# Performance work log

Hardware: AMD Instinct MI355X
Metric: run time of the kernel (lower is better)

## Reference

```python
import jax, jax.numpy as jnp
import numpy as np

N = 50000
E = 800000
D = 128
H = 8
HD = D // H


def setup_inputs() -> dict:
    key = jax.random.key(0)
    ks = jax.random.split(key, 12)
    s = 1.0 / np.sqrt(D)
    x = jax.random.normal(ks[0], (N, D), dtype=jnp.float32)
    edge_index = jax.random.randint(ks[1], (2, E), 0, N, dtype=jnp.int64)
    edge_bias = jax.random.normal(ks[2], (E, H), dtype=jnp.float32)
    Wq = jax.random.uniform(ks[3], (D, D), jnp.float32, -s, s)
    bq = jax.random.uniform(ks[4], (D,), jnp.float32, -s, s)
    Wk = jax.random.uniform(ks[5], (D, D), jnp.float32, -s, s)
    bk = jax.random.uniform(ks[6], (D,), jnp.float32, -s, s)
    Wv = jax.random.uniform(ks[7], (D, D), jnp.float32, -s, s)
    bv = jax.random.uniform(ks[8], (D,), jnp.float32, -s, s)
    Wo = jax.random.uniform(ks[9], (D, D), jnp.float32, -s, s)
    bo = jax.random.uniform(ks[10], (D,), jnp.float32, -s, s)
    return {"x": x, "edge_index": edge_index, "edge_bias": edge_bias,
            "Wq": Wq, "bq": bq, "Wk": Wk, "bk": bk,
            "Wv": Wv, "bv": bv, "Wo": Wo, "bo": bo}


def reference(x, edge_index, edge_bias, Wq, bq, Wk, bk, Wv, bv, Wo, bo):
    scale = HD ** -0.5
    row, col = edge_index[0], edge_index[1]
    # Node-level projections -> [N, H, HD]
    q = (x @ Wq + bq).reshape(N, H, HD)
    k = (x @ Wk + bk).reshape(N, H, HD)
    v = (x @ Wv + bv).reshape(N, H, HD)
    # Edge-level gather + per-edge attention logits [E, H]
    q_i = q[col]
    k_j = k[row]
    v_j = v[row]
    attn = jnp.einsum('ehd,ehd->eh', q_i, k_j) * scale + edge_bias
    # Scatter-softmax over incoming edges of each destination node (col)
    seg_max = jax.ops.segment_max(attn, col, num_segments=N)  # [N, H]
    seg_max = jnp.where(jnp.isfinite(seg_max), seg_max, 0.0)  # empty segments -> 0
    ex = jnp.exp(attn - seg_max[col])
    denom = jax.ops.segment_sum(ex, col, num_segments=N)      # [N, H]
    attn = ex / (denom[col] + 1e-16)
    # Scatter-add weighted values -> [N, H, HD]
    weighted_v = attn[:, :, None] * v_j
    out = jax.ops.segment_sum(weighted_v, col, num_segments=N)
    out = out.reshape(N, D)
    return out @ Wo + bo
```

## Files before the change

kernel.cpp:

```cpp
#include <hip/hip_runtime.h>
#include <math.h>

#define NN 50000
#define EE 800000
#define DD 128
#define HH 8
#define HDD 16
#define CAP 64

typedef __attribute__((ext_vector_type(8))) short short8;
typedef __attribute__((ext_vector_type(4))) float f32x4;

union U8 { ushort u[8]; int4 v; short8 s; };

__device__ __forceinline__ ushort f2bf(float f) {
    uint u = __float_as_uint(f);
    uint r = (u + 0x7fffu + ((u >> 16) & 1u)) >> 16;
    return (ushort)r;
}
__device__ __forceinline__ float bf2f(ushort u) {
    return __uint_as_float(((uint)u) << 16);
}

__global__ void k_prep(const float* __restrict__ Wq, const float* __restrict__ Wk,
                       const float* __restrict__ Wv, const float* __restrict__ Wo,
                       const float* __restrict__ bq, const float* __restrict__ bk,
                       const float* __restrict__ bv, const float* __restrict__ bo,
                       ushort* __restrict__ Wt, float* __restrict__ bpack,
                       int* __restrict__ cursor) {
    if (blockIdx.x < 256) {
        int tid = blockIdx.x * 256 + threadIdx.x;
        int w = tid >> 14, rem = tid & 16383, c = rem >> 7, i = rem & 127;
        const float* W = (w == 0) ? Wq : (w == 1) ? Wk : (w == 2) ? Wv : Wo;
        float s = (w == 0) ? 0.25f : 1.0f;
        Wt[(size_t)w * 16384 + c * 128 + i] = f2bf(W[i * 128 + c] * s);
        if (i == 0) {
            const float* B = (w == 0) ? bq : (w == 1) ? bk : (w == 2) ? bv : bo;
            bpack[w * 128 + c] = B[c] * s;
        }
    } else {
        int i = (blockIdx.x - 256) * 256 + threadIdx.x;
        if (i < NN) cursor[i] = 0;
    }
}

__global__ void k_fill(const int* __restrict__ col, const int* __restrict__ row,
                       int* __restrict__ cursor, int2* __restrict__ reB) {
    int e = blockIdx.x * blockDim.x + threadIdx.x;
    if (e >= EE) return;
    int c = col[e];
    int p = atomicAdd(&cursor[c], 1);
    if (p < CAP) reB[(size_t)c * CAP + p] = make_int2(row[e], e);
}

#define PAD 136

__global__ __launch_bounds__(256) void k_qkv3(
    const float* __restrict__ x, const ushort* __restrict__ Wt,
    const float* __restrict__ bpk,
    ushort* __restrict__ qb, ushort* __restrict__ kk, ushort* __restrict__ vv) {
    __shared__ ushort lA[128 * PAD];
    __shared__ ushort lB[128 * PAD];
    int tid = threadIdx.x;
    int lane = tid & 63, wave = tid >> 6;
    int r0 = blockIdx.x * 128;

#pragma unroll
    for (int it = 0; it < 8; it++) {
        int slot = it * 256 + tid;
        int arow = slot >> 4, c8 = slot & 15;
        int ar = min(r0 + arow, NN - 1);
        const float* xp = x + (size_t)ar * 128 + c8 * 8;
        float4 a = *(const float4*)xp;
        float4 b = *(const float4*)(xp + 4);
        U8 r;
        r.u[0] = f2bf(a.x); r.u[1] = f2bf(a.y); r.u[2] = f2bf(a.z); r.u[3] = f2bf(a.w);
        r.u[4] = f2bf(b.x); r.u[5] = f2bf(b.y); r.u[6] = f2bf(b.z); r.u[7] = f2bf(b.w);
        *(int4*)&lA[arow * PAD + c8 * 8] = r.v;
    }

    int wm = wave >> 1, wn = wave & 1;
    int lr = lane & 15, lg = lane >> 4;

    for (int w = 0; w < 3; w++) {
#pragma unroll
        for (int it = 0; it < 8; it++) {
            int slot = it * 256 + tid;
            int brow = slot >> 4, c16 = slot & 15;
            *(int4*)&lB[brow * PAD + c16 * 8] =
                *(const int4*)&Wt[(size_t)w * 16384 + brow * 128 + c16 * 8];
        }
        __syncthreads();

        f32x4 acc[4][4];
#pragma unroll
        for (int m = 0; m < 4; m++)
#pragma unroll
            for (int n = 0; n < 4; n++) acc[m][n] = (f32x4){0.f, 0.f, 0.f, 0.f};

#pragma unroll
        for (int ks = 0; ks < 4; ks++) {
            short8 a[4], b[4];
#pragma unroll
            for (int m = 0; m < 4; m++)
                a[m] = *(const short8*)&lA[(wm * 64 + m * 16 + lr) * PAD + ks * 32 + lg * 8];
#pragma unroll
            for (int n = 0; n < 4; n++)
                b[n] = *(const short8*)&lB[(wn * 64 + n * 16 + lr) * PAD + ks * 32 + lg * 8];
#pragma unroll
            for (int m = 0; m < 4; m++)
#pragma unroll
                for (int n = 0; n < 4; n++)
                    acc[m][n] = __builtin_amdgcn_mfma_f32_16x16x32_bf16(a[m], b[n], acc[m][n], 0, 0, 0);
        }

#pragma unroll
        for (int n = 0; n < 4; n++) {
            int gcol = wn * 64 + n * 16 + lr;
            float bv_ = bpk[w * 128 + gcol];
#pragma unroll
            for (int m = 0; m < 4; m++) {
#pragma unroll
                for (int rg = 0; rg < 4; rg++) {
                    int grow = r0 + wm * 64 + m * 16 + lg * 4 + rg;
                    if (grow < NN) {
                        float val = acc[m][n][rg] + bv_;
                        ushort h16 = f2bf(val);
                        if (w == 0)      qb[(size_t)grow * 128 + gcol] = h16;
                        else if (w == 1) kk[(size_t)grow * 128 + gcol] = h16;
                        else             vv[(size_t)grow * 128 + gcol] = h16;
                    }
                }
            }
        }
        __syncthreads();
    }
}

__global__ __launch_bounds__(256) void k_gemm128(
    const ushort* __restrict__ A, const ushort* __restrict__ Bt,
    const float* __restrict__ bias, float* __restrict__ Cf, int M) {
    __shared__ ushort lA[128 * PAD];
    __shared__ ushort lB[128 * PAD];
    int tid = threadIdx.x;
    int lane = tid & 63, wave = tid >> 6;
    int r0 = blockIdx.x * 128;

#pragma unroll
    for (int it = 0; it < 8; it++) {
        int slot = it * 256 + tid;
        int row = slot >> 4, c16 = slot & 15;
        int ar = min(r0 + row, M - 1);
        *(int4*)&lA[row * PAD + c16 * 8] = *(const int4*)&A[(size_t)ar * 128 + c16 * 8];
        *(int4*)&lB[row * PAD + c16 * 8] = *(const int4*)&Bt[row * 128 + c16 * 8];
    }
    __syncthreads();

    int wm = wave >> 1, wn = wave & 1;
    int lr = lane & 15, lg = lane >> 4;
    f32x4 acc[4][4];
#pragma unroll
    for (int m = 0; m < 4; m++)
#pragma unroll
        for (int n = 0; n < 4; n++) acc[m][n] = (f32x4){0.f, 0.f, 0.f, 0.f};

#pragma unroll
    for (int ks = 0; ks < 4; ks++) {
        short8 a[4], b[4];
#pragma unroll
        for (int m = 0; m < 4; m++)
            a[m] = *(const short8*)&lA[(wm * 64 + m * 16 + lr) * PAD + ks * 32 + lg * 8];
#pragma unroll
        for (int n = 0; n < 4; n++)
            b[n] = *(const short8*)&lB[(wn * 64 + n * 16 + lr) * PAD + ks * 32 + lg * 8];
#pragma unroll
        for (int m = 0; m < 4; m++)
#pragma unroll
            for (int n = 0; n < 4; n++)
                acc[m][n] = __builtin_amdgcn_mfma_f32_16x16x32_bf16(a[m], b[n], acc[m][n], 0, 0, 0);
    }

#pragma unroll
    for (int n = 0; n < 4; n++) {
        int gcol = wn * 64 + n * 16 + lr;
        float bv_ = bias[gcol];
#pragma unroll
        for (int m = 0; m < 4; m++) {
#pragma unroll
            for (int rg = 0; rg < 4; rg++) {
                int grow = r0 + wm * 64 + m * 16 + lg * 4 + rg;
                if (grow < M) Cf[(size_t)grow * 128 + gcol] = acc[m][n][rg] + bv_;
            }
        }
    }
}

__global__ __launch_bounds__(256) void k_attn(
    const ushort* __restrict__ qb, const ushort* __restrict__ kk,
    const ushort* __restrict__ vv, const float* __restrict__ ebias,
    const int2* __restrict__ reB, const int* __restrict__ deg,
    ushort* __restrict__ aggb) {
    int wave = threadIdx.x >> 6;
    int lane = threadIdx.x & 63;
    int n = blockIdx.x * 4 + wave;
    if (n >= NN) return;
    int cnt = min(deg[n], CAP);
    const int2* bucket = reB + (size_t)n * CAP;
    int h = lane >> 3;
    int j = lane & 7;
    int hb = lane & ~7;

    float qf[16];
    {
        U8 q0, q1;
        const ushort* qp = qb + (size_t)n * DD + h * HDD;
        q0.v = *(const int4*)qp;
        q1.v = *(const int4*)(qp + 8);
#pragma unroll
        for (int t = 0; t < 8; t++) qf[t] = bf2f(q0.u[t]);
#pragma unroll
        for (int t = 0; t < 8; t++) qf[8 + t] = bf2f(q1.u[t]);
    }

    float m = -INFINITY;
    float denom = 0.f;
    float acc0 = 0.f, acc1 = 0.f;

    for (int idx = 0; idx < cnt; idx += 8) {
        int my = idx + j;
        bool valid = my < cnt;
        int2 re = valid ? bucket[my] : make_int2(0, 0);
        int r = re.x;
        float logit = -INFINITY;
        if (valid) {
            const ushort* kp = kk + (size_t)r * DD + h * HDD;
            U8 a0, a1;
            a0.v = *(const int4*)kp;
            a1.v = *(const int4*)(kp + 8);
            float d = 0.f;
#pragma unroll
            for (int t = 0; t < 8; t++) d += qf[t] * bf2f(a0.u[t]);
#pragma unroll
            for (int t = 0; t < 8; t++) d += qf[8 + t] * bf2f(a1.u[t]);
            logit = d + ebias[(size_t)re.y * HH + h];
        }
        float cm = logit;
        cm = fmaxf(cm, __shfl_xor(cm, 1));
        cm = fmaxf(cm, __shfl_xor(cm, 2));
        cm = fmaxf(cm, __shfl_xor(cm, 4));
        float mnew = fmaxf(m, cm);
        float sc = __expf(m - mnew);
        float p = __expf(logit - mnew);
        m = mnew;
        float ps = p;
        ps += __shfl_xor(ps, 1);
        ps += __shfl_xor(ps, 2);
        ps += __shfl_xor(ps, 4);
        denom = denom * sc + ps;
        acc0 *= sc;
        acc1 *= sc;
#pragma unroll
        for (int j2 = 0; j2 < 8; j2++) {
            float pj = __shfl(p, hb + j2);
            int rj = __shfl(r, hb + j2);
            uint vp = *(const uint*)(vv + (size_t)rj * DD + 2 * lane);
            acc0 += pj * bf2f((ushort)(vp & 0xffffu));
            acc1 += pj * bf2f((ushort)(vp >> 16));
        }
    }
    float inv = 1.0f / (denom + 1e-16f);
    uint pack = (uint)f2bf(acc0 * inv) | ((uint)f2bf(acc1 * inv) << 16);
    *(uint*)&aggb[(size_t)n * DD + 2 * lane] = pack;
}

extern "C" void kernel_launch(void* const* d_in, const int* in_sizes, int n_in,
                              void* d_out, int out_size, void* d_ws, size_t ws_size,
                              hipStream_t stream) {
    const float* x     = (const float*)d_in[0];
    const int*   eidx  = (const int*)d_in[1];
    const float* ebias = (const float*)d_in[2];
    const float* Wq    = (const float*)d_in[3];
    const float* bq    = (const float*)d_in[4];
    const float* Wk    = (const float*)d_in[5];
    const float* bk    = (const float*)d_in[6];
    const float* Wv    = (const float*)d_in[7];
    const float* bv    = (const float*)d_in[8];
    const float* Wo    = (const float*)d_in[9];
    const float* bo    = (const float*)d_in[10];
    float* out = (float*)d_out;

    const int* row = eidx;
    const int* col = eidx + EE;

    char* p = (char*)d_ws;
    ushort* qb    = (ushort*)p;  p += (size_t)NN * DD * 2;
    ushort* kk    = (ushort*)p;  p += (size_t)NN * DD * 2;
    ushort* vvp   = (ushort*)p;  p += (size_t)NN * DD * 2;
    ushort* aggb  = (ushort*)p;  p += (size_t)NN * DD * 2;
    ushort* Wt    = (ushort*)p;  p += (size_t)4 * 16384 * 2;
    float*  bpk   = (float*)p;   p += 4 * 128 * 4;
    int2*   reB   = (int2*)p;    p += (size_t)NN * CAP * 8;
    int* cursor   = (int*)p;     p += (size_t)NN * 4;

    const int SCB = (NN + 255) / 256;

    hipLaunchKernelGGL(k_prep, dim3(256 + SCB), dim3(256), 0, stream,
                       Wq, Wk, Wv, Wo, bq, bk, bv, bo, Wt, bpk, cursor);
    hipLaunchKernelGGL(k_fill, dim3((EE + 255) / 256), dim3(256), 0, stream,
                       col, row, cursor, reB);

    const int GB = (NN + 127) / 128;
    hipLaunchKernelGGL(k_qkv3, dim3(GB), dim3(256), 0, stream,
                       x, Wt, bpk, qb, kk, vvp);

    hipLaunchKernelGGL(k_attn, dim3(NN / 4), dim3(256), 0, stream,
                       qb, kk, vvp, ebias, reB, cursor, aggb);

    hipLaunchKernelGGL(k_gemm128, dim3(GB), dim3(256), 0, stream,
                       aggb, Wt + 3 * 16384, bpk + 3 * 128, out, NN);
}
```

Before: 212.4 us.

## Fuse edge bucketing into QKV GEMM and output projection into attention

Edge bucketing (atomic fill) now runs as extra blocks of the QKV projection kernel instead of a separate launch. The output projection by Wo is fused into the attention kernel: each block stages Wo as bf16 in LDS and runs a persistent loop over nodes, doing a per-node 128x128 matvec with scalar FMAs from LDS. This removes two launches and the aggb round trip, but replaces an MFMA GEMM with scalar matvec work per node and caps the attention grid at 1024 persistent blocks, which may lower occupancy for the latency-bound gather.

```diff
diff --git a/kernel.cpp b/kernel.cpp
--- a/kernel.cpp
+++ b/kernel.cpp
@@ -7,6 +7,10 @@
 #define HH 8
 #define HDD 16
 #define CAP 64
+#define GB 391
+#define FILLB 3125
+#define PAD 136
+#define WOP 132
 
 typedef __attribute__((ext_vector_type(8))) short short8;
 typedef __attribute__((ext_vector_type(4))) float f32x4;
@@ -23,45 +27,47 @@
 }
 
 __global__ void k_prep(const float* __restrict__ Wq, const float* __restrict__ Wk,
-                       const float* __restrict__ Wv, const float* __restrict__ Wo,
+                       const float* __restrict__ Wv,
                        const float* __restrict__ bq, const float* __restrict__ bk,
-                       const float* __restrict__ bv, const float* __restrict__ bo,
+                       const float* __restrict__ bv,
                        ushort* __restrict__ Wt, float* __restrict__ bpack,
                        int* __restrict__ cursor) {
-    if (blockIdx.x < 256) {
+    if (blockIdx.x < 192) {
         int tid = blockIdx.x * 256 + threadIdx.x;
         int w = tid >> 14, rem = tid & 16383, c = rem >> 7, i = rem & 127;
-        const float* W = (w == 0) ? Wq : (w == 1) ? Wk : (w == 2) ? Wv : Wo;
+        const float* W = (w == 0) ? Wq : (w == 1) ? Wk : Wv;
         float s = (w == 0) ? 0.25f : 1.0f;
         Wt[(size_t)w * 16384 + c * 128 + i] = f2bf(W[i * 128 + c] * s);
         if (i == 0) {
-            const float* B = (w == 0) ? bq : (w == 1) ? bk : (w == 2) ? bv : bo;
+            const float* B = (w == 0) ? bq : (w == 1) ? bk : bv;
             bpack[w * 128 + c] = B[c] * s;
         }
     } else {
-        int i = (blockIdx.x - 256) * 256 + threadIdx.x;
+        int i = (blockIdx.x - 192) * 256 + threadIdx.x;
         if (i < NN) cursor[i] = 0;
     }
 }
 
-__global__ void k_fill(const int* __restrict__ col, const int* __restrict__ row,
-                       int* __restrict__ cursor, int2* __restrict__ reB) {
-    int e = blockIdx.x * blockDim.x + threadIdx.x;
-    if (e >= EE) return;
-    int c = col[e];
-    int p = atomicAdd(&cursor[c], 1);
-    if (p < CAP) reB[(size_t)c * CAP + p] = make_int2(row[e], e);
-}
-
-#define PAD 136
-
-__global__ __launch_bounds__(256) void k_qkv3(
+__global__ __launch_bounds__(256) void k_main(
     const float* __restrict__ x, const ushort* __restrict__ Wt,
     const float* __restrict__ bpk,
-    ushort* __restrict__ qb, ushort* __restrict__ kk, ushort* __restrict__ vv) {
+    ushort* __restrict__ qb, ushort* __restrict__ kk, ushort* __restrict__ vv,
+    const int* __restrict__ col, const int* __restrict__ row,
+    int* __restrict__ cursor, int2* __restrict__ reB) {
     __shared__ ushort lA[128 * PAD];
     __shared__ ushort lB[128 * PAD];
     int tid = threadIdx.x;
+
+    if (blockIdx.x >= GB) {
+        int e = (blockIdx.x - GB) * 256 + tid;
+        if (e < EE) {
+            int c = col[e];
+            int p = atomicAdd(&cursor[c], 1);
+            if (p < CAP) reB[(size_t)c * CAP + p] = make_int2(row[e], e);
+        }
+        return;
+    }
+
     int lane = tid & 63, wave = tid >> 6;
     int r0 = blockIdx.x * 128;
 
@@ -137,140 +143,109 @@
     }
 }
 
-__global__ __launch_bounds__(256) void k_gemm128(
-    const ushort* __restrict__ A, const ushort* __restrict__ Bt,
-    const float* __restrict__ bias, float* __restrict__ Cf, int M) {
-    __shared__ ushort lA[128 * PAD];
-    __shared__ ushort lB[128 * PAD];
-    int tid = threadIdx.x;
-    int lane = tid & 63, wave = tid >> 6;
-    int r0 = blockIdx.x * 128;
-
-#pragma unroll
-    for (int it = 0; it < 8; it++) {
-        int slot = it * 256 + tid;
-        int row = slot >> 4, c16 = slot & 15;
-        int ar = min(r0 + row, M - 1);
-        *(int4*)&lA[row * PAD + c16 * 8] = *(const int4*)&A[(size_t)ar * 128 + c16 * 8];
-        *(int4*)&lB[row * PAD + c16 * 8] = *(const int4*)&Bt[row * 128 + c16 * 8];
-    }
-    __syncthreads();
-
-    int wm = wave >> 1, wn = wave & 1;
-    int lr = lane & 15, lg = lane >> 4;
-    f32x4 acc[4][4];
-#pragma unroll
-    for (int m = 0; m < 4; m++)
-#pragma unroll
-        for (int n = 0; n < 4; n++) acc[m][n] = (f32x4){0.f, 0.f, 0.f, 0.f};
-
-#pragma unroll
-    for (int ks = 0; ks < 4; ks++) {
-        short8 a[4], b[4];
-#pragma unroll
-        for (int m = 0; m < 4; m++)
-            a[m] = *(const short8*)&lA[(wm * 64 + m * 16 + lr) * PAD + ks * 32 + lg * 8];
-#pragma unroll
-        for (int n = 0; n < 4; n++)
-            b[n] = *(const short8*)&lB[(wn * 64 + n * 16 + lr) * PAD + ks * 32 + lg * 8];
-#pragma unroll
-        for (int m = 0; m < 4; m++)
-#pragma unroll
-            for (int n = 0; n < 4; n++)
-                acc[m][n] = __builtin_amdgcn_mfma_f32_16x16x32_bf16(a[m], b[n], acc[m][n], 0, 0, 0);
-    }
-
-#pragma unroll
-    for (int n = 0; n < 4; n++) {
-        int gcol = wn * 64 + n * 16 + lr;
-        float bv_ = bias[gcol];
-#pragma unroll
-        for (int m = 0; m < 4; m++) {
-#pragma unroll
-            for (int rg = 0; rg < 4; rg++) {
-                int grow = r0 + wm * 64 + m * 16 + lg * 4 + rg;
-                if (grow < M) Cf[(size_t)grow * 128 + gcol] = acc[m][n][rg] + bv_;
-            }
-        }
-    }
-}
-
 __global__ __launch_bounds__(256) void k_attn(
     const ushort* __restrict__ qb, const ushort* __restrict__ kk,
     const ushort* __restrict__ vv, const float* __restrict__ ebias,
     const int2* __restrict__ reB, const int* __restrict__ deg,
-    ushort* __restrict__ aggb) {
-    int wave = threadIdx.x >> 6;
-    int lane = threadIdx.x & 63;
-    int n = blockIdx.x * 4 + wave;
-    if (n >= NN) return;
-    int cnt = min(deg[n], CAP);
-    const int2* bucket = reB + (size_t)n * CAP;
+    const float* __restrict__ Wo, const float* __restrict__ bo,
+    float* __restrict__ out) {
+    __shared__ ushort lWo[128 * WOP];
+    __shared__ float lag[4][128];
+    int tid = threadIdx.x;
+
+#pragma unroll
+    for (int it = 0; it < 32; it++) {
+        int idx = it * 512 + tid * 2;
+        float2 w2 = *(const float2*)&Wo[idx];
+        uint pk = (uint)f2bf(w2.x) | ((uint)f2bf(w2.y) << 16);
+        int i = idx >> 7, c = idx & 127;
+        *(uint*)&lWo[i * WOP + c] = pk;
+    }
+    __syncthreads();
+
+    int wave = tid >> 6;
+    int lane = tid & 63;
     int h = lane >> 3;
     int j = lane & 7;
     int hb = lane & ~7;
-
-    float qf[16];
-    {
-        U8 q0, q1;
-        const ushort* qp = qb + (size_t)n * DD + h * HDD;
-        q0.v = *(const int4*)qp;
-        q1.v = *(const int4*)(qp + 8);
-#pragma unroll
-        for (int t = 0; t < 8; t++) qf[t] = bf2f(q0.u[t]);
-#pragma unroll
-        for (int t = 0; t < 8; t++) qf[8 + t] = bf2f(q1.u[t]);
-    }
-
-    float m = -INFINITY;
-    float denom = 0.f;
-    float acc0 = 0.f, acc1 = 0.f;
-
-    for (int idx = 0; idx < cnt; idx += 8) {
-        int my = idx + j;
-        bool valid = my < cnt;
-        int2 re = valid ? bucket[my] : make_int2(0, 0);
-        int r = re.x;
-        float logit = -INFINITY;
-        if (valid) {
-            const ushort* kp = kk + (size_t)r * DD + h * HDD;
-            U8 a0, a1;
-            a0.v = *(const int4*)kp;
-            a1.v = *(const int4*)(kp + 8);
-            float d = 0.f;
-#pragma unroll
-            for (int t = 0; t < 8; t++) d += qf[t] * bf2f(a0.u[t]);
-#pragma unroll
-            for (int t = 0; t < 8; t++) d += qf[8 + t] * bf2f(a1.u[t]);
-            logit = d + ebias[(size_t)re.y * HH + h];
-        }
-        float cm = logit;
-        cm = fmaxf(cm, __shfl_xor(cm, 1));
-        cm = fmaxf(cm, __shfl_xor(cm, 2));
-        cm = fmaxf(cm, __shfl_xor(cm, 4));
-        float mnew = fmaxf(m, cm);
-        float sc = __expf(m - mnew);
-        float p = __expf(logit - mnew);
-        m = mnew;
-        float ps = p;
-        ps += __shfl_xor(ps, 1);
-        ps += __shfl_xor(ps, 2);
-        ps += __shfl_xor(ps, 4);
-        denom = denom * sc + ps;
-        acc0 *= sc;
-        acc1 *= sc;
-#pragma unroll
-        for (int j2 = 0; j2 < 8; j2++) {
-            float pj = __shfl(p, hb + j2);
-            int rj = __shfl(r, hb + j2);
-            uint vp = *(const uint*)(vv + (size_t)rj * DD + 2 * lane);
-            acc0 += pj * bf2f((ushort)(vp & 0xffffu));
-            acc1 += pj * bf2f((ushort)(vp >> 16));
-        }
-    }
-    float inv = 1.0f / (denom + 1e-16f);
-    uint pack = (uint)f2bf(acc0 * inv) | ((uint)f2bf(acc1 * inv) << 16);
-    *(uint*)&aggb[(size_t)n * DD + 2 * lane] = pack;
+    float bo0 = bo[2 * lane], bo1 = bo[2 * lane + 1];
+
+    for (int n = blockIdx.x * 4 + wave; n < NN; n += 4096) {
+        int cnt = min(deg[n], CAP);
+        const int2* bucket = reB + (size_t)n * CAP;
+
+        float qf[16];
+        {
+            U8 q0, q1;
+            const ushort* qp = qb + (size_t)n * DD + h * HDD;
+            q0.v = *(const int4*)qp;
+            q1.v = *(const int4*)(qp + 8);
+#pragma unroll
+            for (int t = 0; t < 8; t++) qf[t] = bf2f(q0.u[t]);
+#pragma unroll
+            for (int t = 0; t < 8; t++) qf[8 + t] = bf2f(q1.u[t]);
+        }
+
+        float m = -INFINITY;
+        float denom = 0.f;
+        float acc0 = 0.f, acc1 = 0.f;
+
+        for (int idx = 0; idx < cnt; idx += 8) {
+            int my = idx + j;
+            bool valid = my < cnt;
+            int2 re = valid ? bucket[my] : make_int2(0, 0);
+            int r = re.x;
+            float logit = -INFINITY;
+            if (valid) {
+                const ushort* kp = kk + (size_t)r * DD + h * HDD;
+                U8 a0, a1;
+                a0.v = *(const int4*)kp;
+                a1.v = *(const int4*)(kp + 8);
+                float d = 0.f;
+#pragma unroll
+                for (int t = 0; t < 8; t++) d += qf[t] * bf2f(a0.u[t]);
+#pragma unroll
+                for (int t = 0; t < 8; t++) d += qf[8 + t] * bf2f(a1.u[t]);
+                logit = d + ebias[(size_t)re.y * HH + h];
+            }
+            float cm = logit;
+            cm = fmaxf(cm, __shfl_xor(cm, 1));
+            cm = fmaxf(cm, __shfl_xor(cm, 2));
+            cm = fmaxf(cm, __shfl_xor(cm, 4));
+            float mnew = fmaxf(m, cm);
+            float sc = __expf(m - mnew);
+            float p = __expf(logit - mnew);
+            m = mnew;
+            float ps = p;
+            ps += __shfl_xor(ps, 1);
+            ps += __shfl_xor(ps, 2);
+            ps += __shfl_xor(ps, 4);
+            denom = denom * sc + ps;
+            acc0 *= sc;
+            acc1 *= sc;
+#pragma unroll
+            for (int j2 = 0; j2 < 8; j2++) {
+                float pj = __shfl(p, hb + j2);
+                int rj = __shfl(r, hb + j2);
+                uint vp = *(const uint*)(vv + (size_t)rj * DD + 2 * lane);
+                acc0 += pj * bf2f((ushort)(vp & 0xffffu));
+                acc1 += pj * bf2f((ushort)(vp >> 16));
+            }
+        }
+        float inv = 1.0f / (denom + 1e-16f);
+        lag[wave][2 * lane]     = acc0 * inv;
+        lag[wave][2 * lane + 1] = acc1 * inv;
+
+        float s0 = bo0, s1 = bo1;
+#pragma unroll 4
+        for (int i = 0; i < 128; i++) {
+            float a = lag[wave][i];
+            uint w2 = *(const uint*)&lWo[i * WOP + 2 * lane];
+            s0 += a * bf2f((ushort)(w2 & 0xffffu));
+            s1 += a * bf2f((ushort)(w2 >> 16));
+        }
+        *(float2*)&out[(size_t)n * DD + 2 * lane] = make_float2(s0, s1);
+    }
 }
 
 extern "C" void kernel_launch(void* const* d_in, const int* in_sizes, int n_in,
@@ -296,26 +271,19 @@
     ushort* qb    = (ushort*)p;  p += (size_t)NN * DD * 2;
     ushort* kk    = (ushort*)p;  p += (size_t)NN * DD * 2;
     ushort* vvp   = (ushort*)p;  p += (size_t)NN * DD * 2;
-    ushort* aggb  = (ushort*)p;  p += (size_t)NN * DD * 2;
-    ushort* Wt    = (ushort*)p;  p += (size_t)4 * 16384 * 2;
-    float*  bpk   = (float*)p;   p += 4 * 128 * 4;
+    ushort* Wt    = (ushort*)p;  p += (size_t)3 * 16384 * 2;
+    float*  bpk   = (float*)p;   p += 3 * 128 * 4;
     int2*   reB   = (int2*)p;    p += (size_t)NN * CAP * 8;
     int* cursor   = (int*)p;     p += (size_t)NN * 4;
 
     const int SCB = (NN + 255) / 256;
 
-    hipLaunchKernelGGL(k_prep, dim3(256 + SCB), dim3(256), 0, stream,
-                       Wq, Wk, Wv, Wo, bq, bk, bv, bo, Wt, bpk, cursor);
-    hipLaunchKernelGGL(k_fill, dim3((EE + 255) / 256), dim3(256), 0, stream,
-                       col, row, cursor, reB);
-
-    const int GB = (NN + 127) / 128;
-    hipLaunchKernelGGL(k_qkv3, dim3(GB), dim3(256), 0, stream,
-                       x, Wt, bpk, qb, kk, vvp);
-
-    hipLaunchKernelGGL(k_attn, dim3(NN / 4), dim3(256), 0, stream,
-                       qb, kk, vvp, ebias, reB, cursor, aggb);
-
-    hipLaunchKernelGGL(k_gemm128, dim3(GB), dim3(256), 0, stream,
-                       aggb, Wt + 3 * 16384, bpk + 3 * 128, out, NN);
-}
+    hipLaunchKernelGGL(k_prep, dim3(192 + SCB), dim3(256), 0, stream,
+                       Wq, Wk, Wv, bq, bk, bv, Wt, bpk, cursor);
+
+    hipLaunchKernelGGL(k_main, dim3(GB + FILLB), dim3(256), 0, stream,
+                       x, Wt, bpk, qb, kk, vvp, col, row, cursor, reB);
+
+    hipLaunchKernelGGL(k_attn, dim3(1024), dim3(256), 0, stream,
+                       qb, kk, vvp, ebias, reB, cursor, Wo, bo, out);
+}
```

After: 196.8 us. 1.08x faster.

## Read GEMM weights and activations directly from global memory instead of LDS staging

Applied to the files above, without the earlier changes.

The QKV and output GEMM kernels no longer stage the weight tile (and, for the output GEMM, the activation tile) through shared memory. MFMA operands are loaded straight from global memory, and the per-iteration barriers go away. The cursor zeroing moves from the prep kernel to a hipMemsetAsync call. The aim is to cut LDS traffic, barriers and LDS footprint so occupancy can rise. In exchange, every wave issues redundant, less coalesced global loads that depend on L1/L2 hits, and the output GEMM loses its LDS reuse of A.

```diff
diff --git a/kernel.cpp b/kernel.cpp
--- a/kernel.cpp
+++ b/kernel.cpp
@@ -7,6 +7,8 @@
 #define HH 8
 #define HDD 16
 #define CAP 64
+#define GB 391
+#define PAD 136
 
 typedef __attribute__((ext_vector_type(8))) short short8;
 typedef __attribute__((ext_vector_type(4))) float f32x4;
@@ -26,41 +28,32 @@
                        const float* __restrict__ Wv, const float* __restrict__ Wo,
                        const float* __restrict__ bq, const float* __restrict__ bk,
                        const float* __restrict__ bv, const float* __restrict__ bo,
-                       ushort* __restrict__ Wt, float* __restrict__ bpack,
-                       int* __restrict__ cursor) {
-    if (blockIdx.x < 256) {
-        int tid = blockIdx.x * 256 + threadIdx.x;
-        int w = tid >> 14, rem = tid & 16383, c = rem >> 7, i = rem & 127;
-        const float* W = (w == 0) ? Wq : (w == 1) ? Wk : (w == 2) ? Wv : Wo;
-        float s = (w == 0) ? 0.25f : 1.0f;
-        Wt[(size_t)w * 16384 + c * 128 + i] = f2bf(W[i * 128 + c] * s);
-        if (i == 0) {
-            const float* B = (w == 0) ? bq : (w == 1) ? bk : (w == 2) ? bv : bo;
-            bpack[w * 128 + c] = B[c] * s;
-        }
-    } else {
-        int i = (blockIdx.x - 256) * 256 + threadIdx.x;
-        if (i < NN) cursor[i] = 0;
+                       ushort* __restrict__ Wt, float* __restrict__ bpack) {
+    int tid = blockIdx.x * 256 + threadIdx.x;
+    int w = tid >> 14, rem = tid & 16383, c = rem >> 7, i = rem & 127;
+    const float* W = (w == 0) ? Wq : (w == 1) ? Wk : (w == 2) ? Wv : Wo;
+    float s = (w == 0) ? 0.25f : 1.0f;
+    Wt[(size_t)w * 16384 + c * 128 + i] = f2bf(W[i * 128 + c] * s);
+    if (i == 0) {
+        const float* B = (w == 0) ? bq : (w == 1) ? bk : (w == 2) ? bv : bo;
+        bpack[w * 128 + c] = B[c] * s;
     }
 }
 
 __global__ void k_fill(const int* __restrict__ col, const int* __restrict__ row,
                        int* __restrict__ cursor, int2* __restrict__ reB) {
-    int e = blockIdx.x * blockDim.x + threadIdx.x;
+    int e = blockIdx.x * 256 + threadIdx.x;
     if (e >= EE) return;
     int c = col[e];
     int p = atomicAdd(&cursor[c], 1);
     if (p < CAP) reB[(size_t)c * CAP + p] = make_int2(row[e], e);
 }
-
-#define PAD 136
 
 __global__ __launch_bounds__(256) void k_qkv3(
     const float* __restrict__ x, const ushort* __restrict__ Wt,
     const float* __restrict__ bpk,
     ushort* __restrict__ qb, ushort* __restrict__ kk, ushort* __restrict__ vv) {
     __shared__ ushort lA[128 * PAD];
-    __shared__ ushort lB[128 * PAD];
     int tid = threadIdx.x;
     int lane = tid & 63, wave = tid >> 6;
     int r0 = blockIdx.x * 128;
@@ -78,20 +71,12 @@
         r.u[4] = f2bf(b.x); r.u[5] = f2bf(b.y); r.u[6] = f2bf(b.z); r.u[7] = f2bf(b.w);
         *(int4*)&lA[arow * PAD + c8 * 8] = r.v;
     }
+    __syncthreads();
 
     int wm = wave >> 1, wn = wave & 1;
     int lr = lane & 15, lg = lane >> 4;
 
     for (int w = 0; w < 3; w++) {
-#pragma unroll
-        for (int it = 0; it < 8; it++) {
-            int slot = it * 256 + tid;
-            int brow = slot >> 4, c16 = slot & 15;
-            *(int4*)&lB[brow * PAD + c16 * 8] =
-                *(const int4*)&Wt[(size_t)w * 16384 + brow * 128 + c16 * 8];
-        }
-        __syncthreads();
-
         f32x4 acc[4][4];
 #pragma unroll
         for (int m = 0; m < 4; m++)
@@ -106,7 +91,8 @@
                 a[m] = *(const short8*)&lA[(wm * 64 + m * 16 + lr) * PAD + ks * 32 + lg * 8];
 #pragma unroll
             for (int n = 0; n < 4; n++)
-                b[n] = *(const short8*)&lB[(wn * 64 + n * 16 + lr) * PAD + ks * 32 + lg * 8];
+                b[n] = *(const short8*)&Wt[(size_t)w * 16384 +
+                                           (wn * 64 + n * 16 + lr) * 128 + ks * 32 + lg * 8];
 #pragma unroll
             for (int m = 0; m < 4; m++)
 #pragma unroll
@@ -133,31 +119,18 @@
                 }
             }
         }
-        __syncthreads();
     }
 }
 
 __global__ __launch_bounds__(256) void k_gemm128(
     const ushort* __restrict__ A, const ushort* __restrict__ Bt,
     const float* __restrict__ bias, float* __restrict__ Cf, int M) {
-    __shared__ ushort lA[128 * PAD];
-    __shared__ ushort lB[128 * PAD];
     int tid = threadIdx.x;
     int lane = tid & 63, wave = tid >> 6;
     int r0 = blockIdx.x * 128;
-
-#pragma unroll
-    for (int it = 0; it < 8; it++) {
-        int slot = it * 256 + tid;
-        int row = slot >> 4, c16 = slot & 15;
-        int ar = min(r0 + row, M - 1);
-        *(int4*)&lA[row * PAD + c16 * 8] = *(const int4*)&A[(size_t)ar * 128 + c16 * 8];
-        *(int4*)&lB[row * PAD + c16 * 8] = *(const int4*)&Bt[row * 128 + c16 * 8];
-    }
-    __syncthreads();
-
     int wm = wave >> 1, wn = wave & 1;
     int lr = lane & 15, lg = lane >> 4;
+
     f32x4 acc[4][4];
 #pragma unroll
     for (int m = 0; m < 4; m++)
@@ -168,11 +141,13 @@
     for (int ks = 0; ks < 4; ks++) {
         short8 a[4], b[4];
 #pragma unroll
-        for (int m = 0; m < 4; m++)
-            a[m] = *(const short8*)&lA[(wm * 64 + m * 16 + lr) * PAD + ks * 32 + lg * 8];
+        for (int m = 0; m < 4; m++) {
+            int ar = min(r0 + wm * 64 + m * 16 + lr, M - 1);
+            a[m] = *(const short8*)&A[(size_t)ar * 128 + ks * 32 + lg * 8];
+        }
 #pragma unroll
         for (int n = 0; n < 4; n++)
-            b[n] = *(const short8*)&lB[(wn * 64 + n * 16 + lr) * PAD + ks * 32 + lg * 8];
+            b[n] = *(const short8*)&Bt[(wn * 64 + n * 16 + lr) * 128 + ks * 32 + lg * 8];
 #pragma unroll
         for (int m = 0; m < 4; m++)
 #pragma unroll
@@ -302,14 +277,14 @@
     int2*   reB   = (int2*)p;    p += (size_t)NN * CAP * 8;
     int* cursor   = (int*)p;     p += (size_t)NN * 4;
 
-    const int SCB = (NN + 255) / 256;
-
-    hipLaunchKernelGGL(k_prep, dim3(256 + SCB), dim3(256), 0, stream,
-                       Wq, Wk, Wv, Wo, bq, bk, bv, bo, Wt, bpk, cursor);
-    hipLaunchKernelGGL(k_fill, dim3((EE + 255) / 256), dim3(256), 0, stream,
+    hipMemsetAsync(cursor, 0, (size_t)NN * sizeof(int), stream);
+
+    hipLaunchKernelGGL(k_prep, dim3(256), dim3(256), 0, stream,
+                       Wq, Wk, Wv, Wo, bq, bk, bv, bo, Wt, bpk);
+
+    hipLaunchKernelGGL(k_fill, dim3(EE / 256), dim3(256), 0, stream,
                        col, row, cursor, reB);
 
-    const int GB = (NN + 127) / 128;
     hipLaunchKernelGGL(k_qkv3, dim3(GB), dim3(256), 0, stream,
                        x, Wt, bpk, qb, kk, vvp);
 
```

After: 218.0 us. +2.7%, slower.
